# Kernel tuning notes

Hardware: AMD Instinct MI355X
Metric: run time of the kernel (lower is better)

The kernel has to match this reference:

```python
import jax, jax.numpy as jnp
import numpy as np

NUM_LAYERS = 32
IN_SIZE = 1024
OUT_SIZE = 1024
B, S = 32, 256


def setup_inputs() -> dict:
    key = jax.random.key(0)
    k1, k2, k3 = jax.random.split(key, 3)
    x = jax.random.normal(k1, (B, S, IN_SIZE), dtype=jnp.float32)
    layer_idx = jax.random.randint(k2, (S,), 0, NUM_LAYERS, dtype=jnp.int32)
    # learned parameter: per-layer weight [L, O, D], normal(stddev=1.0) as in flax init
    weight = jax.random.normal(k3, (NUM_LAYERS, OUT_SIZE, IN_SIZE), dtype=jnp.float32)
    return {"x": x, "layer_idx": layer_idx, "weight": weight}


def reference(x, layer_idx, weight):
    # x: [B, S, D]; layer_idx: [S]; weight: [L, O, D]
    # Each sequence position s uses expert weight[layer_idx[s]]:
    #   out[b, s, o] = sum_d x[b, s, d] * weight[layer_idx[s], o, d]
    w = weight[layer_idx]                      # [S, O, D] gather
    return jnp.einsum('bsd,sod->bso', x, w)    # [B, S, O]
```

## Files before the change

kernel.cpp:

```cpp
#include <hip/hip_runtime.h>
#include <stdint.h>

#define NLAYERS 32
#define DSIZE   1024
#define OSIZE   1024
#define BATCH   32
#define SEQ     256

#define WS_PERM  16
#define WS_TILE  512
#define CHUNK    8
#define MAXC     60
#define BK       64
#define TM       256
#define TN       256
#define THREADS  512

typedef __attribute__((ext_vector_type(8)))  short short8;
typedef __attribute__((ext_vector_type(16))) float f32x16;
typedef __attribute__((ext_vector_type(4)))  unsigned uint4v;

__global__ void prep_kernel(const int* __restrict__ layer_idx, int* __restrict__ wsi) {
    __shared__ int cnt[NLAYERS];
    __shared__ int start_[NLAYERS];
    __shared__ int cursor[NLAYERS];
    const int t = threadIdx.x;
    if (t < NLAYERS) cnt[t] = 0;
    __syncthreads();
    int l = 0;
    if (t < SEQ) { l = layer_idx[t]; atomicAdd(&cnt[l], 1); }
    __syncthreads();
    if (t == 0) {
        int acc = 0;
        for (int i = 0; i < NLAYERS; ++i) { start_[i] = acc; cursor[i] = acc; acc += cnt[i]; }
    }
    __syncthreads();
    if (t < SEQ) {
        int r = atomicAdd(&cursor[l], 1);
        wsi[WS_PERM + r] = t;
    }
    if (t == 0) {
        int nc = 0;
        for (int i = 0; i < NLAYERS; ++i) {
            const int c = cnt[i];
            for (int j = 0; j < c; j += CHUNK) {
                wsi[WS_TILE + nc*4 + 0] = i;
                wsi[WS_TILE + nc*4 + 1] = start_[i] + j;
                wsi[WS_TILE + nc*4 + 2] = (c - j < CHUNK) ? (c - j) : CHUNK;
                ++nc;
            }
        }
        wsi[0] = nc;
    }
}

static __device__ __forceinline__ unsigned pk2(float a, float b) {
    unsigned ua = __builtin_bit_cast(unsigned, a) + 0x8000u;
    unsigned ub = __builtin_bit_cast(unsigned, b) + 0x8000u;
    return __builtin_amdgcn_perm(ub, ua, 0x07060302u);
}

__global__ __launch_bounds__(THREADS, 2) void gemm_kernel(
        const float* __restrict__ x, const float* __restrict__ wgt,
        const int* __restrict__ wsi, float* __restrict__ out) {
    const int fid = blockIdx.x;
    const int g     = (fid & 7) | ((fid >> 5) << 3);
    const int ntile = (fid >> 3) & 3;
    const int nchunks = wsi[0];
    if (g >= nchunks) return;
    const int layer     = wsi[WS_TILE + g*4 + 0];
    const int rank_base = wsi[WS_TILE + g*4 + 1];
    const int nranks    = wsi[WS_TILE + g*4 + 2];

    __shared__ __align__(16) short ldsA[TM * BK];
    __shared__ __align__(16) short ldsB[TN * BK];

    const int t    = threadIdx.x;
    const int slot = t & 7;
    const int rb   = t >> 3;
    const int wsw  = ((slot ^ (rb & 7)) << 3);

    const float* aptr[4];
    bool av[4];
    #pragma unroll
    for (int p = 0; p < 4; ++p) {
        const int r  = rb + 64*p;
        const int ro = r >> 5;
        const int b  = r & 31;
        av[p] = (ro < nranks);
        const int s = av[p] ? wsi[WS_PERM + rank_base + ro] : 0;
        aptr[p] = x + (((size_t)(b * SEQ + s)) << 10) + slot*8;
    }
    const float* bptr = wgt + ((size_t)layer << 20)
                            + (((size_t)(ntile * TN + rb)) << 10) + slot*8;

    float4 ra[4][2], rbv[4][2];
    auto load_step = [&](int kk) {
        #pragma unroll
        for (int p = 0; p < 4; ++p) {
            if (av[p]) {
                ra[p][0] = *(const float4*)(aptr[p] + kk);
                ra[p][1] = *(const float4*)(aptr[p] + kk + 4);
            }
        }
        #pragma unroll
        for (int p = 0; p < 4; ++p) {
            rbv[p][0] = *(const float4*)(bptr + ((size_t)p << 16) + kk);
            rbv[p][1] = *(const float4*)(bptr + ((size_t)p << 16) + kk + 4);
        }
    };

    const int lane = t & 63;
    const int wv   = t >> 6;
    const int l31  = lane & 31;
    const int lh   = lane >> 5;
    const int wm   = (wv >> 1) * 64;
    const int wn   = (wv & 1) * 128;
    const int rsw  = l31 & 7;

    const int baseA0 = (wm +  0 + l31) * BK;
    const int baseA1 = (wm + 32 + l31) * BK;
    int baseB[4];
    #pragma unroll
    for (int ni = 0; ni < 4; ++ni) baseB[ni] = (wn + ni*32 + l31) * BK;

    const int rank0 = wm >> 5;
    const bool ok0 = (rank0 + 0) < nranks;
    const bool ok1 = (rank0 + 1) < nranks;

    f32x16 acc[2][4];
    #pragma unroll
    for (int mi = 0; mi < 2; ++mi)
        #pragma unroll
        for (int ni = 0; ni < 4; ++ni)
            #pragma unroll
            for (int r = 0; r < 16; ++r) acc[mi][ni][r] = 0.f;

    load_step(0);
    #pragma unroll 1
    for (int kk = 0; kk < DSIZE; kk += BK) {
        __syncthreads();
        #pragma unroll
        for (int p = 0; p < 4; ++p) {
            if (av[p]) {
                uint4v u;
                u.x = pk2(ra[p][0].x, ra[p][0].y);
                u.y = pk2(ra[p][0].z, ra[p][0].w);
                u.z = pk2(ra[p][1].x, ra[p][1].y);
                u.w = pk2(ra[p][1].z, ra[p][1].w);
                *(uint4v*)&ldsA[(rb + 64*p) * BK + wsw] = u;
            }
        }
        #pragma unroll
        for (int p = 0; p < 4; ++p) {
            uint4v u;
            u.x = pk2(rbv[p][0].x, rbv[p][0].y);
            u.y = pk2(rbv[p][0].z, rbv[p][0].w);
            u.z = pk2(rbv[p][1].x, rbv[p][1].y);
            u.w = pk2(rbv[p][1].z, rbv[p][1].w);
            *(uint4v*)&ldsB[(rb + 64*p) * BK + wsw] = u;
        }
        __syncthreads();
        if (kk + BK < DSIZE) load_step(kk + BK);
        if (ok0) {
            #pragma unroll
            for (int sub = 0; sub < 4; ++sub) {
                const int gx = (((sub*2 + lh) ^ rsw) << 3);
                short8 b0[4];
                #pragma unroll
                for (int ni = 0; ni < 4; ++ni)
                    b0[ni] = *(const short8*)&ldsB[baseB[ni] + gx];
                {
                    short8 a0 = *(const short8*)&ldsA[baseA0 + gx];
                    #pragma unroll
                    for (int ni = 0; ni < 4; ++ni)
                        acc[0][ni] = __builtin_amdgcn_mfma_f32_32x32x16_bf16(a0, b0[ni], acc[0][ni], 0, 0, 0);
                }
                if (ok1) {
                    short8 a1 = *(const short8*)&ldsA[baseA1 + gx];
                    #pragma unroll
                    for (int ni = 0; ni < 4; ++ni)
                        acc[1][ni] = __builtin_amdgcn_mfma_f32_32x32x16_bf16(a1, b0[ni], acc[1][ni], 0, 0, 0);
                }
            }
        }
    }

    #pragma unroll
    for (int mi = 0; mi < 2; ++mi) {
        const int ro = rank0 + mi;
        if (ro < nranks) {
            const int s = wsi[WS_PERM + rank_base + ro];
            #pragma unroll
            for (int ni = 0; ni < 4; ++ni) {
                const int ocol = ntile * TN + wn + ni*32 + l31;
                #pragma unroll
                for (int r = 0; r < 16; ++r) {
                    const int brow = (r & 3) + 8*(r >> 2) + 4*lh;
                    out[(((size_t)(brow * SEQ + s)) << 10) + ocol] = acc[mi][ni][r];
                }
            }
        }
    }
}

extern "C" void kernel_launch(void* const* d_in, const int* in_sizes, int n_in,
                              void* d_out, int out_size, void* d_ws, size_t ws_size,
                              hipStream_t stream) {
    const float* x         = (const float*)d_in[0];
    const int*   layer_idx = (const int*)  d_in[1];
    const float* weight    = (const float*)d_in[2];
    float* out = (float*)d_out;
    int*   wsi = (int*)d_ws;

    prep_kernel<<<1, 256, 0, stream>>>(layer_idx, wsi);
    gemm_kernel<<<256, THREADS, 0, stream>>>(x, weight, wsi, out);
}
```

Before: 260.2 us.

## Double-buffer LDS and halve N tile to double grid parallelism

```diff
diff --git a/kernel.cpp b/kernel.cpp
--- a/kernel.cpp
+++ b/kernel.cpp
@@ -10,11 +10,11 @@
 #define WS_PERM  16
 #define WS_TILE  512
 #define CHUNK    8
-#define MAXC     60
-#define BK       64
+#define BK       32
 #define TM       256
-#define TN       256
+#define TN       128
 #define THREADS  512
+#define KITERS   (DSIZE / BK)
 
 typedef __attribute__((ext_vector_type(8)))  short short8;
 typedef __attribute__((ext_vector_type(16))) float f32x16;
@@ -60,31 +60,33 @@
     return __builtin_amdgcn_perm(ub, ua, 0x07060302u);
 }
 
-__global__ __launch_bounds__(THREADS, 2) void gemm_kernel(
+__global__ __launch_bounds__(THREADS, 4) void gemm_kernel(
         const float* __restrict__ x, const float* __restrict__ wgt,
         const int* __restrict__ wsi, float* __restrict__ out) {
     const int fid = blockIdx.x;
-    const int g     = (fid & 7) | ((fid >> 5) << 3);
-    const int ntile = (fid >> 3) & 3;
+    const int xcd = fid & 7;
+    const int u   = fid >> 3;
+    const int g   = ((u >> 3) << 3) | xcd;
+    const int ntile = u & 7;
     const int nchunks = wsi[0];
     if (g >= nchunks) return;
     const int layer     = wsi[WS_TILE + g*4 + 0];
     const int rank_base = wsi[WS_TILE + g*4 + 1];
     const int nranks    = wsi[WS_TILE + g*4 + 2];
 
-    __shared__ __align__(16) short ldsA[TM * BK];
-    __shared__ __align__(16) short ldsB[TN * BK];
+    __shared__ __align__(16) short ldsA[2][TM * BK];
+    __shared__ __align__(16) short ldsB[2][TN * BK];
 
     const int t    = threadIdx.x;
-    const int slot = t & 7;
-    const int rb   = t >> 3;
-    const int wsw  = ((slot ^ (rb & 7)) << 3);
-
-    const float* aptr[4];
-    bool av[4];
+    const int slot = t & 3;
+    const int rb   = t >> 2;
+    const int wsw  = ((slot ^ (rb & 3)) << 3);
+
+    const float* aptr[2];
+    bool av[2];
     #pragma unroll
-    for (int p = 0; p < 4; ++p) {
-        const int r  = rb + 64*p;
+    for (int p = 0; p < 2; ++p) {
+        const int r  = rb + 128*p;
         const int ro = r >> 5;
         const int b  = r & 31;
         av[p] = (ro < nranks);
@@ -94,19 +96,37 @@
     const float* bptr = wgt + ((size_t)layer << 20)
                             + (((size_t)(ntile * TN + rb)) << 10) + slot*8;
 
-    float4 ra[4][2], rbv[4][2];
+    float4 ra[2][2], rbv[2];
     auto load_step = [&](int kk) {
         #pragma unroll
-        for (int p = 0; p < 4; ++p) {
+        for (int p = 0; p < 2; ++p) {
             if (av[p]) {
                 ra[p][0] = *(const float4*)(aptr[p] + kk);
                 ra[p][1] = *(const float4*)(aptr[p] + kk + 4);
             }
         }
-        #pragma unroll
-        for (int p = 0; p < 4; ++p) {
-            rbv[p][0] = *(const float4*)(bptr + ((size_t)p << 16) + kk);
-            rbv[p][1] = *(const float4*)(bptr + ((size_t)p << 16) + kk + 4);
+        rbv[0] = *(const float4*)(bptr + kk);
+        rbv[1] = *(const float4*)(bptr + kk + 4);
+    };
+    auto store_to = [&](int buf) {
+        #pragma unroll
+        for (int p = 0; p < 2; ++p) {
+            if (av[p]) {
+                uint4v u4;
+                u4.x = pk2(ra[p][0].x, ra[p][0].y);
+                u4.y = pk2(ra[p][0].z, ra[p][0].w);
+                u4.z = pk2(ra[p][1].x, ra[p][1].y);
+                u4.w = pk2(ra[p][1].z, ra[p][1].w);
+                *(uint4v*)&ldsA[buf][(rb + 128*p) * BK + wsw] = u4;
+            }
+        }
+        {
+            uint4v u4;
+            u4.x = pk2(rbv[0].x, rbv[0].y);
+            u4.y = pk2(rbv[0].z, rbv[0].w);
+            u4.z = pk2(rbv[1].x, rbv[1].y);
+            u4.w = pk2(rbv[1].z, rbv[1].w);
+            *(uint4v*)&ldsB[buf][rb * BK + wsw] = u4;
         }
     };
 
@@ -114,75 +134,55 @@
     const int wv   = t >> 6;
     const int l31  = lane & 31;
     const int lh   = lane >> 5;
-    const int wm   = (wv >> 1) * 64;
-    const int wn   = (wv & 1) * 128;
-    const int rsw  = l31 & 7;
+    const int wm   = (wv >> 1) << 6;
+    const int wn   = (wv & 1) << 6;
+    const int rsw  = l31 & 3;
 
     const int baseA0 = (wm +  0 + l31) * BK;
     const int baseA1 = (wm + 32 + l31) * BK;
-    int baseB[4];
-    #pragma unroll
-    for (int ni = 0; ni < 4; ++ni) baseB[ni] = (wn + ni*32 + l31) * BK;
+    const int baseB0 = (wn +  0 + l31) * BK;
+    const int baseB1 = (wn + 32 + l31) * BK;
 
     const int rank0 = wm >> 5;
     const bool ok0 = (rank0 + 0) < nranks;
     const bool ok1 = (rank0 + 1) < nranks;
 
-    f32x16 acc[2][4];
+    f32x16 acc[2][2];
     #pragma unroll
     for (int mi = 0; mi < 2; ++mi)
         #pragma unroll
-        for (int ni = 0; ni < 4; ++ni)
+        for (int ni = 0; ni < 2; ++ni)
             #pragma unroll
             for (int r = 0; r < 16; ++r) acc[mi][ni][r] = 0.f;
 
     load_step(0);
+    store_to(0);
+    __syncthreads();
+
     #pragma unroll 1
-    for (int kk = 0; kk < DSIZE; kk += BK) {
-        __syncthreads();
-        #pragma unroll
-        for (int p = 0; p < 4; ++p) {
-            if (av[p]) {
-                uint4v u;
-                u.x = pk2(ra[p][0].x, ra[p][0].y);
-                u.y = pk2(ra[p][0].z, ra[p][0].w);
-                u.z = pk2(ra[p][1].x, ra[p][1].y);
-                u.w = pk2(ra[p][1].z, ra[p][1].w);
-                *(uint4v*)&ldsA[(rb + 64*p) * BK + wsw] = u;
-            }
-        }
-        #pragma unroll
-        for (int p = 0; p < 4; ++p) {
-            uint4v u;
-            u.x = pk2(rbv[p][0].x, rbv[p][0].y);
-            u.y = pk2(rbv[p][0].z, rbv[p][0].w);
-            u.z = pk2(rbv[p][1].x, rbv[p][1].y);
-            u.w = pk2(rbv[p][1].z, rbv[p][1].w);
-            *(uint4v*)&ldsB[(rb + 64*p) * BK + wsw] = u;
-        }
-        __syncthreads();
-        if (kk + BK < DSIZE) load_step(kk + BK);
-        if (ok0) {
-            #pragma unroll
-            for (int sub = 0; sub < 4; ++sub) {
-                const int gx = (((sub*2 + lh) ^ rsw) << 3);
-                short8 b0[4];
-                #pragma unroll
-                for (int ni = 0; ni < 4; ++ni)
-                    b0[ni] = *(const short8*)&ldsB[baseB[ni] + gx];
-                {
-                    short8 a0 = *(const short8*)&ldsA[baseA0 + gx];
-                    #pragma unroll
-                    for (int ni = 0; ni < 4; ++ni)
-                        acc[0][ni] = __builtin_amdgcn_mfma_f32_32x32x16_bf16(a0, b0[ni], acc[0][ni], 0, 0, 0);
-                }
-                if (ok1) {
-                    short8 a1 = *(const short8*)&ldsA[baseA1 + gx];
-                    #pragma unroll
-                    for (int ni = 0; ni < 4; ++ni)
-                        acc[1][ni] = __builtin_amdgcn_mfma_f32_32x32x16_bf16(a1, b0[ni], acc[1][ni], 0, 0, 0);
-                }
-            }
+    for (int kt = 0; kt < KITERS; ++kt) {
+        const int cur = kt & 1;
+        const bool more = (kt + 1 < KITERS);
+        if (more) load_step((kt + 1) * BK);
+        #pragma unroll
+        for (int sub = 0; sub < 2; ++sub) {
+            const int gx = (((sub << 1) | lh) ^ rsw) << 3;
+            short8 b0 = *(const short8*)&ldsB[cur][baseB0 + gx];
+            short8 b1 = *(const short8*)&ldsB[cur][baseB1 + gx];
+            if (ok0) {
+                short8 a0 = *(const short8*)&ldsA[cur][baseA0 + gx];
+                acc[0][0] = __builtin_amdgcn_mfma_f32_32x32x16_bf16(a0, b0, acc[0][0], 0, 0, 0);
+                acc[0][1] = __builtin_amdgcn_mfma_f32_32x32x16_bf16(a0, b1, acc[0][1], 0, 0, 0);
+            }
+            if (ok1) {
+                short8 a1 = *(const short8*)&ldsA[cur][baseA1 + gx];
+                acc[1][0] = __builtin_amdgcn_mfma_f32_32x32x16_bf16(a1, b0, acc[1][0], 0, 0, 0);
+                acc[1][1] = __builtin_amdgcn_mfma_f32_32x32x16_bf16(a1, b1, acc[1][1], 0, 0, 0);
+            }
+        }
+        if (more) {
+            store_to(cur ^ 1);
+            __syncthreads();
         }
     }
 
@@ -192,7 +192,7 @@
         if (ro < nranks) {
             const int s = wsi[WS_PERM + rank_base + ro];
             #pragma unroll
-            for (int ni = 0; ni < 4; ++ni) {
+            for (int ni = 0; ni < 2; ++ni) {
                 const int ocol = ntile * TN + wn + ni*32 + l31;
                 #pragma unroll
                 for (int r = 0; r < 16; ++r) {
@@ -214,5 +214,5 @@
     int*   wsi = (int*)d_ws;
 
     prep_kernel<<<1, 256, 0, stream>>>(layer_idx, wsi);
-    gemm_kernel<<<256, THREADS, 0, stream>>>(x, weight, wsi, out);
-}
+    gemm_kernel<<<512, THREADS, 0, stream>>>(x, weight, wsi, out);
+}
```

Result: slower. 275.2 us (+5.8%).
